# Optimization experiments

Measured on AMD Instinct MI355X. Metric: run time of the kernel, lower is better.

## Reference

```python
import jax, jax.numpy as jnp
import numpy as np

SEQ_LEN = 96      # args.seq_len (in_feats)
H_FEATS = 100
OUT_FEATS = 128
HEADS = 4
K = 64            # args.input_size = nodes per graph
B = 256           # number of graphs (batch_size)
N = K * B
DEG = 8
E = N * DEG
OUT_SIZE = 24     # args.output_size
NEG_SLOPE = 0.2   # PyG GATConv default


def setup_inputs() -> dict:
    key = jax.random.key(0)
    ks = jax.random.split(key, 20)
    s = 0.05
    x = jax.random.normal(ks[0], (N, SEQ_LEN), jnp.float32)
    # intra-graph random edges (dst repeated, src within same graph)
    dst = jnp.repeat(jnp.arange(N, dtype=jnp.int32), DEG)
    src = (dst // K) * K + jax.random.randint(ks[1], (E,), 0, K, dtype=jnp.int32)
    edge_index = jnp.stack([src, dst])
    batch = jnp.repeat(jnp.arange(B, dtype=jnp.int32), K)
    y = jax.random.normal(ks[2], (N, OUT_SIZE), jnp.float32)
    # GATConv 1: in=96 -> heads=4, ch=100
    W1 = jax.random.normal(ks[3], (SEQ_LEN, HEADS * H_FEATS), jnp.float32) * s
    as1 = jax.random.normal(ks[4], (HEADS, H_FEATS), jnp.float32) * s
    ad1 = jax.random.normal(ks[5], (HEADS, H_FEATS), jnp.float32) * s
    b1 = jnp.zeros((H_FEATS,), jnp.float32)
    # GATConv 2: in=100 -> heads=4, ch=128
    W2 = jax.random.normal(ks[6], (H_FEATS, HEADS * OUT_FEATS), jnp.float32) * s
    as2 = jax.random.normal(ks[7], (HEADS, OUT_FEATS), jnp.float32) * s
    ad2 = jax.random.normal(ks[8], (HEADS, OUT_FEATS), jnp.float32) * s
    b2 = jnp.zeros((OUT_FEATS,), jnp.float32)
    # per-node-index MLPs (batched over K)
    fw1 = jax.random.normal(ks[9], (K, OUT_FEATS, 64), jnp.float32) * s
    fb1 = jnp.zeros((K, 64), jnp.float32)
    fw2 = jax.random.normal(ks[10], (K, 64, OUT_SIZE), jnp.float32) * s
    fb2 = jnp.zeros((K, OUT_SIZE), jnp.float32)
    return dict(x=x, edge_index=edge_index, batch=batch, y=y,
                W1=W1, as1=as1, ad1=ad1, b1=b1,
                W2=W2, as2=as2, ad2=ad2, b2=b2,
                fw1=fw1, fb1=fb1, fw2=fw2, fb2=fb2)


def gat_conv(x, src, dst, W, a_src, a_dst, bias):
    # PyG GATConv (concat=False): linear -> per-edge attention -> softmax over
    # incoming edges of each dst -> weighted sum -> mean over heads + bias.
    n = x.shape[0]
    xl = (x @ W).reshape(n, HEADS, -1)                      # [N,H,C]
    al_src = jnp.sum(xl * a_src, axis=-1)                   # [N,H]
    al_dst = jnp.sum(xl * a_dst, axis=-1)                   # [N,H]
    alpha = jax.nn.leaky_relu(al_src[src] + al_dst[dst], NEG_SLOPE)  # [E,H]
    m = jax.ops.segment_max(alpha, dst, num_segments=n)
    ea = jnp.exp(alpha - m[dst])
    denom = jax.ops.segment_sum(ea, dst, num_segments=n)
    w = ea / (denom[dst] + 1e-16)                           # [E,H]
    msg = xl[src] * w[:, :, None]                           # [E,H,C]
    out = jax.ops.segment_sum(msg, dst, num_segments=n)     # [N,H,C]
    return out.mean(axis=1) + bias                          # concat=False


def reference(x, edge_index, batch, y, W1, as1, ad1, b1, W2, as2, ad2, b2, fw1, fb1, fw2, fb2):
    n = x.shape[0]
    src, dst = edge_index[0], edge_index[1]
    loop = jnp.arange(n, dtype=src.dtype)                   # GATConv adds self-loops
    src = jnp.concatenate([src, loop])
    dst = jnp.concatenate([dst, loop])
    h = jax.nn.elu(gat_conv(x, src, dst, W1, as1, ad1, b1))
    h = gat_conv(h, src, dst, W2, as2, ad2, b2)             # [N,128]
    # batch is sorted with K nodes per graph -> stacking == static reshape
    xg = h.reshape(B, K, OUT_FEATS).transpose(1, 0, 2)      # [K,B,128]
    hid = jax.nn.relu(jnp.einsum('kbi,kih->kbh', xg, fw1) + fb1[:, None, :])
    pred = jnp.einsum('kbh,kho->kbo', hid, fw2) + fb2[:, None, :]  # [K,B,out]
    yg = y.reshape(B, K, OUT_SIZE)                          # [B,K,out]
    return pred, yg
```

## Files before the change

### kernel.cpp

```cpp
#include <hip/hip_runtime.h>
#include <hip/hip_bf16.h>
#include <math.h>


#define N_NODES 16384
#define B_GRAPHS 256
#define K_NODES 64
#define DEG 8
#define NHEADS 4
#define C1 100
#define C2 128
#define IN_F 96
#define HID 64
#define OUT_SZ 24
#define PRED_ELEMS (K_NODES * B_GRAPHS * OUT_SZ)

#define W1T_ROWS 448
#define W1T_K    96
#define W2T_ROWS 512
#define W2T_K    128

using bf16 = __hip_bfloat16;
typedef __attribute__((ext_vector_type(8))) short          frag_ab;
typedef __attribute__((ext_vector_type(4))) float          frag_cd;
typedef unsigned short us8 __attribute__((ext_vector_type(8)));
typedef unsigned short us4 __attribute__((ext_vector_type(4)));

__device__ __forceinline__ float us2f(unsigned short u) {
  return __bfloat162float(__ushort_as_bfloat16(u));
}
__device__ __forceinline__ short f2bf_s(float f) {
  return __builtin_bit_cast(short, __float2bfloat16(f));
}

#define P1N (W1T_ROWS * W1T_K)
#define P2N (W2T_ROWS * W2T_K)
#define YG4 (PRED_ELEMS / 4)

__global__ __launch_bounds__(256)
void prep(const float* __restrict__ W1, const float* __restrict__ W2,
          const float* __restrict__ y,
          bf16* __restrict__ W1t, bf16* __restrict__ W2t,
          float* __restrict__ yg) {
  int idx = blockIdx.x * 256 + threadIdx.x;
  if (idx < P1N) {
    int c = idx / W1T_K, k = idx - c * W1T_K;
    W1t[idx] = __float2bfloat16((c < 400) ? W1[(size_t)k * 400 + c] : 0.f);
  } else if (idx < P1N + P2N) {
    int i2 = idx - P1N;
    int c = i2 >> 7, k = i2 & 127;
    W2t[i2] = __float2bfloat16((k < 100) ? W2[(size_t)k * 512 + c] : 0.f);
  } else {
    int j = idx - P1N - P2N;
    if (j < YG4) {
      int i = j * 4;
      float4 v = *(const float4*)(y + i);
      v.x = __bfloat162float(__float2bfloat16(v.x));
      v.y = __bfloat162float(__float2bfloat16(v.y));
      v.z = __bfloat162float(__float2bfloat16(v.z));
      v.w = __bfloat162float(__float2bfloat16(v.w));
      *(float4*)(yg + i) = v;
    }
  }
}

__global__ __launch_bounds__(512)
void gat_fused(const float* __restrict__ x,
               const bf16* __restrict__ W1t, const bf16* __restrict__ W2t,
               const int* __restrict__ esrc,
               const float* __restrict__ as1, const float* __restrict__ ad1,
               const float* __restrict__ b1,
               const float* __restrict__ as2, const float* __restrict__ ad2,
               const float* __restrict__ b2,
               bf16* __restrict__ h2out) {
  constexpr int LDA1 = IN_F + 8;
  constexpr int LDA2 = 136;
  constexpr int LDT  = 72;

  __shared__ __align__(16) short          As[64 * LDA2];
  __shared__ __align__(16) unsigned short xs[512 * LDT];
  __shared__ __align__(16) short          Ps[NHEADS * 64 * LDT];
  __shared__ float avs1[400], avd1[400], avs2[512], avd2[512];
  __shared__ float bia1[C1], bia2[C2];
  __shared__ int   edg[K_NODES * DEG];
  __shared__ float als[64 * 5], ald[64 * 5];

  const int g = blockIdx.x;
  const int t = threadIdx.x;
  const int wv = t >> 6;
  const int l  = t & 63;
  const int lm = l & 15;
  const int lk = (l >> 4) * 8;
  const int rq = (l >> 4) * 4;

  {
    constexpr int QR = IN_F / 4;
    for (int idx = t; idx < 64 * QR; idx += 512) {
      int m = idx / QR, q = idx - m * QR;
      const float4 v = *(const float4*)(x + ((size_t)(g * 64 + m) * IN_F + q * 4));
      short* d = &As[m * LDA1 + q * 4];
      d[0] = f2bf_s(v.x); d[1] = f2bf_s(v.y); d[2] = f2bf_s(v.z); d[3] = f2bf_s(v.w);
    }
  }
  for (int idx = t; idx < 400; idx += 512) { avs1[idx] = as1[idx]; avd1[idx] = ad1[idx]; }
  for (int idx = t; idx < 512; idx += 512) { avs2[idx] = as2[idx]; avd2[idx] = ad2[idx]; }
  if (t < C1) bia1[t] = b1[t];
  if (t < C2) bia2[t] = b2[t];
  if (t < K_NODES * DEG) edg[t] = esrc[g * K_NODES * DEG + t] & (K_NODES - 1);
  for (int idx = t; idx < NHEADS * 64 * LDT / 8; idx += 512)
    *(us8*)&Ps[idx * 8] = (us8)0;
  __syncthreads();

  if (wv < 7) {
    const int n0 = wv * 64;
    frag_cd acc[4][4] = {};
#pragma unroll
    for (int ks = 0; ks < IN_F; ks += 32) {
      frag_ab b[4];
#pragma unroll
      for (int nt = 0; nt < 4; ++nt)
        b[nt] = *(const frag_ab*)((const short*)W1t +
                                  (size_t)(n0 + nt * 16 + lm) * W1T_K + ks + lk);
#pragma unroll
      for (int mt = 0; mt < 4; ++mt) {
        frag_ab a = *(const frag_ab*)&As[(mt * 16 + lm) * LDA1 + ks + lk];
#pragma unroll
        for (int nt = 0; nt < 4; ++nt)
          acc[mt][nt] = __builtin_amdgcn_mfma_f32_16x16x32_bf16(a, b[nt],
                                                                acc[mt][nt], 0, 0, 0);
      }
    }
#pragma unroll
    for (int mt = 0; mt < 4; ++mt)
#pragma unroll
      for (int nt = 0; nt < 4; ++nt) {
        const int c4 = n0 + nt * 16 + lm;
        us4 o;
#pragma unroll
        for (int r = 0; r < 4; ++r) o[r] = (unsigned short)f2bf_s(acc[mt][nt][r]);
        *(us4*)&xs[c4 * LDT + mt * 16 + rq] = o;
      }
  }
  __syncthreads();

  if (t < 256) {
    const int n = t >> 2, h = t & 3;
    float ss = 0.f, sd = 0.f;
#pragma unroll 4
    for (int c = 0; c < C1; ++c) {
      const float v = us2f(xs[(h * C1 + c) * LDT + n]);
      ss += v * avs1[h * C1 + c];
      sd += v * avd1[h * C1 + c];
    }
    als[n * 5 + h] = ss;
    ald[n * 5 + h] = sd;
  }
  __syncthreads();

  if (t < 256) {
    const int n = t >> 2, h = t & 3;
    const float ad = ald[n * 5 + h];
    int   sv[9];
    float a[9];
#pragma unroll
    for (int j = 0; j < 8; ++j) sv[j] = edg[n * DEG + j];
    sv[8] = n;
#pragma unroll
    for (int j = 0; j < 9; ++j) {
      float v = als[sv[j] * 5 + h] + ad;
      a[j] = (v >= 0.f) ? v : 0.2f * v;
    }
    float m = -1e30f;
#pragma unroll
    for (int j = 0; j < 9; ++j) m = fmaxf(m, a[j]);
    float s = 0.f;
#pragma unroll
    for (int j = 0; j < 9; ++j) { a[j] = __expf(a[j] - m); s += a[j]; }
    const float inv = 1.f / (s + 1e-16f);
    short* prow = &Ps[(h * 64 + n) * LDT];
#pragma unroll
    for (int j = 0; j < 9; ++j) {
      float tw = a[j];
#pragma unroll
      for (int i = 0; i < 9; ++i)
        if (i != j && sv[i] == sv[j]) tw += a[i];
      prow[sv[j]] = f2bf_s(tw * inv);
    }
  } else {
    for (int i = t - 256; i < 64 * 28; i += 256) {
      int m = i / 28, kk = 100 + (i - m * 28);
      As[m * LDA2 + kk] = 0;
    }
  }
  __syncthreads();

  {
    const int mw = (wv & 3) * 16;
    const int cg = wv >> 2;
    const int ntb = cg * 4;
    const int nte = (cg == 0) ? 4 : 7;
    frag_cd acc[4] = {};
#pragma unroll
    for (int h = 0; h < NHEADS; ++h)
#pragma unroll
      for (int ks = 0; ks < 64; ks += 32) {
        frag_ab a = *(const frag_ab*)&Ps[(h * 64 + mw + lm) * LDT + ks + lk];
        for (int nt = ntb; nt < nte; ++nt) {
          frag_ab b = *(const frag_ab*)&xs[(h * C1 + nt * 16 + lm) * LDT + ks + lk];
          acc[nt - ntb] = __builtin_amdgcn_mfma_f32_16x16x32_bf16(a, b,
                                                                  acc[nt - ntb], 0, 0, 0);
      }
    }
    for (int nt = ntb; nt < nte; ++nt) {
      const int c = nt * 16 + lm;
      if (c < C1) {
        const float bc = bia1[c];
#pragma unroll
        for (int r = 0; r < 4; ++r) {
          float vv = acc[nt - ntb][r] * 0.25f + bc;
          vv = (vv > 0.f) ? vv : (__expf(vv) - 1.f);
          As[(mw + rq + r) * LDA2 + c] = f2bf_s(vv);
        }
      }
    }
  }
  __syncthreads();

  {
    const int n0 = wv * 64;
    frag_cd acc[4][4] = {};
#pragma unroll
    for (int ks = 0; ks < 128; ks += 32) {
      frag_ab b[4];
#pragma unroll
      for (int nt = 0; nt < 4; ++nt)
        b[nt] = *(const frag_ab*)((const short*)W2t +
                                  (size_t)(n0 + nt * 16 + lm) * W2T_K + ks + lk);
#pragma unroll
      for (int mt = 0; mt < 4; ++mt) {
        frag_ab a = *(const frag_ab*)&As[(mt * 16 + lm) * LDA2 + ks + lk];
#pragma unroll
        for (int nt = 0; nt < 4; ++nt)
          acc[mt][nt] = __builtin_amdgcn_mfma_f32_16x16x32_bf16(a, b[nt],
                                                                acc[mt][nt], 0, 0, 0);
      }
    }
#pragma unroll
    for (int mt = 0; mt < 4; ++mt)
#pragma unroll
      for (int nt = 0; nt < 4; ++nt) {
        const int c4 = n0 + nt * 16 + lm;
        us4 o;
#pragma unroll
        for (int r = 0; r < 4; ++r) o[r] = (unsigned short)f2bf_s(acc[mt][nt][r]);
        *(us4*)&xs[c4 * LDT + mt * 16 + rq] = o;
      }
  }
  __syncthreads();

  if (t < 256) {
    const int n = t >> 2, h = t & 3;
    float ss = 0.f, sd = 0.f;
#pragma unroll 4
    for (int c = 0; c < C2; ++c) {
      const float v = us2f(xs[(h * C2 + c) * LDT + n]);
      ss += v * avs2[h * C2 + c];
      sd += v * avd2[h * C2 + c];
    }
    als[n * 5 + h] = ss;
    ald[n * 5 + h] = sd;
  }
  __syncthreads();

  if (t < 256) {
    const int n = t >> 2, h = t & 3;
    const float ad = ald[n * 5 + h];
    int   sv[9];
    float a[9];
#pragma unroll
    for (int j = 0; j < 8; ++j) sv[j] = edg[n * DEG + j];
    sv[8] = n;
#pragma unroll
    for (int j = 0; j < 9; ++j) {
      float v = als[sv[j] * 5 + h] + ad;
      a[j] = (v >= 0.f) ? v : 0.2f * v;
    }
    float m = -1e30f;
#pragma unroll
    for (int j = 0; j < 9; ++j) m = fmaxf(m, a[j]);
    float s = 0.f;
#pragma unroll
    for (int j = 0; j < 9; ++j) { a[j] = __expf(a[j] - m); s += a[j]; }
    const float inv = 1.f / (s + 1e-16f);
    short* prow = &Ps[(h * 64 + n) * LDT];
#pragma unroll
    for (int j = 0; j < 9; ++j) {
      float tw = a[j];
#pragma unroll
      for (int i = 0; i < 9; ++i)
        if (i != j && sv[i] == sv[j]) tw += a[i];
      prow[sv[j]] = f2bf_s(tw * inv);
    }
  }
  __syncthreads();

  {
    const int mw = (wv & 3) * 16;
    const int cg = wv >> 2;
    const int ntb = cg * 4;
    frag_cd acc[4] = {};
#pragma unroll
    for (int h = 0; h < NHEADS; ++h)
#pragma unroll
      for (int ks = 0; ks < 64; ks += 32) {
        frag_ab a = *(const frag_ab*)&Ps[(h * 64 + mw + lm) * LDT + ks + lk];
#pragma unroll
        for (int nt = 0; nt < 4; ++nt) {
          frag_ab b = *(const frag_ab*)&xs[(h * C2 + (ntb + nt) * 16 + lm) * LDT + ks + lk];
          acc[nt] = __builtin_amdgcn_mfma_f32_16x16x32_bf16(a, b, acc[nt], 0, 0, 0);
        }
      }
    unsigned short* outp = (unsigned short*)h2out + (size_t)(g * 64) * C2;
#pragma unroll
    for (int nt = 0; nt < 4; ++nt) {
      const int c = (ntb + nt) * 16 + lm;
      const float bc = bia2[c];
#pragma unroll
      for (int r = 0; r < 4; ++r) {
        float vv = acc[nt][r] * 0.25f + bc;
        outp[(size_t)(mw + rq + r) * C2 + c] = (unsigned short)f2bf_s(vv);
      }
    }
  }
}

__global__ __launch_bounds__(256)
void mlp_mfma(const bf16* __restrict__ h2,
              const float* __restrict__ fw1, const float* __restrict__ fb1,
              const float* __restrict__ fw2, const float* __restrict__ fb2,
              float* __restrict__ pred) {
  constexpr int LDA = C2 + 8;
  constexpr int LDH = HID + 8;
  __shared__ __align__(16) short As[64 * LDA];
  __shared__ __align__(16) short B1[HID * LDA];
  __shared__ __align__(16) short Hs[64 * LDH];
  __shared__ __align__(16) short B2[32 * LDH];
  __shared__ float b1s[HID];
  __shared__ float b2s[32];

  const int k  = blockIdx.x & 63;
  const int ms = blockIdx.x >> 6;
  const int t  = threadIdx.x;

  for (int idx = t; idx < 64 * 16; idx += 256) {
    int r = idx >> 4, o = idx & 15;
    const us8 v = *(const us8*)((const unsigned short*)h2 +
        ((size_t)((ms * 64 + r) * K_NODES + k) * C2) + o * 8);
    *(us8*)&As[r * LDA + o * 8] = v;
  }
  for (int idx = t; idx < C2 * HID; idx += 256) {
    int kk = idx >> 6, n = idx & 63;
    B1[n * LDA + kk] = f2bf_s(fw1[(size_t)k * C2 * HID + kk * HID + n]);
  }
  for (int idx = t; idx < HID * 32; idx += 256) {
    int kk = idx >> 5, n = idx & 31;
    float v = (n < OUT_SZ) ? fw2[(size_t)k * HID * OUT_SZ + kk * OUT_SZ + n] : 0.f;
    B2[n * LDH + kk] = f2bf_s(v);
  }
  if (t < HID) b1s[t] = fb1[k * HID + t];
  if (t < 32)  b2s[t] = (t < OUT_SZ) ? fb2[k * OUT_SZ + t] : 0.f;
  __syncthreads();

  const int wv = t >> 6;
  const int l  = t & 63;
  const int lm = l & 15;
  const int lk = (l >> 4) * 8;
  const int rq = (l >> 4) * 4;

  frag_cd acc[4] = {};
#pragma unroll
  for (int ks = 0; ks < C2; ks += 32) {
    frag_ab a = *(const frag_ab*)&As[(wv * 16 + lm) * LDA + ks + lk];
#pragma unroll
    for (int nt = 0; nt < 4; ++nt) {
      frag_ab b = *(const frag_ab*)&B1[(nt * 16 + lm) * LDA + ks + lk];
      acc[nt] = __builtin_amdgcn_mfma_f32_16x16x32_bf16(a, b, acc[nt], 0, 0, 0);
    }
  }
#pragma unroll
  for (int nt = 0; nt < 4; ++nt) {
    const int j  = nt * 16 + lm;
    const float bj = b1s[j];
#pragma unroll
    for (int r = 0; r < 4; ++r) {
      const int m = wv * 16 + rq + r;
      Hs[m * LDH + j] = f2bf_s(fmaxf(acc[nt][r] + bj, 0.f));
    }
  }
  __syncthreads();

  frag_cd acc2[2] = {};
#pragma unroll
  for (int ks = 0; ks < HID; ks += 32) {
    frag_ab a = *(const frag_ab*)&Hs[(wv * 16 + lm) * LDH + ks + lk];
#pragma unroll
    for (int nt = 0; nt < 2; ++nt) {
      frag_ab b = *(const frag_ab*)&B2[(nt * 16 + lm) * LDH + ks + lk];
      acc2[nt] = __builtin_amdgcn_mfma_f32_16x16x32_bf16(a, b, acc2[nt], 0, 0, 0);
    }
  }
#pragma unroll
  for (int nt = 0; nt < 2; ++nt) {
    const int q = nt * 16 + lm;
    if (q < OUT_SZ) {
      const float bq = b2s[q];
#pragma unroll
      for (int r = 0; r < 4; ++r) {
        const int m = wv * 16 + rq + r;
        pred[((size_t)k * B_GRAPHS + ms * 64 + m) * OUT_SZ + q] = acc2[nt][r] + bq;
      }
    }
  }
}

extern "C" void kernel_launch(void* const* d_in, const int* in_sizes, int n_in,
                              void* d_out, int out_size, void* d_ws, size_t ws_size,
                              hipStream_t stream) {
  const float* x   = (const float*)d_in[0];
  const int*   ei  = (const int*)d_in[1];
  const float* y   = (const float*)d_in[3];
  const float* W1  = (const float*)d_in[4];
  const float* as1 = (const float*)d_in[5];
  const float* ad1 = (const float*)d_in[6];
  const float* b1  = (const float*)d_in[7];
  const float* W2  = (const float*)d_in[8];
  const float* as2 = (const float*)d_in[9];
  const float* ad2 = (const float*)d_in[10];
  const float* b2  = (const float*)d_in[11];
  const float* fw1 = (const float*)d_in[12];
  const float* fb1 = (const float*)d_in[13];
  const float* fw2 = (const float*)d_in[14];
  const float* fb2 = (const float*)d_in[15];

  bf16* h2  = (bf16*)d_ws;
  bf16* W1t = h2 + (size_t)N_NODES * C2;
  bf16* W2t = W1t + P1N;

  float* out = (float*)d_out;

  prep<<<(P1N + P2N + YG4 + 255) / 256, 256, 0, stream>>>(
      W1, W2, y, W1t, W2t, out + PRED_ELEMS);

  gat_fused<<<B_GRAPHS, 512, 0, stream>>>(x, W1t, W2t, ei,
                                          as1, ad1, b1, as2, ad2, b2, h2);

  mlp_mfma<<<K_NODES * 4, 256, 0, stream>>>(h2, fw1, fb1, fw2, fb2, out);
}
```

Baseline: 119.4 us.

## Fold attention vectors into weight GEMMs and pre-transpose MLP weights to bf16

Precomputes W·a_src and W·a_dst as extra columns appended to the transposed weight matrices, so the attention logits come out of the existing MFMA GEMMs. This replaces the separate per-node dot-product loops and two block barriers per layer. The MLP weights are converted and transposed to bf16 once in the prep kernel. The GAT output is written in a [K,B,C] layout so the MLP kernel reads A and B fragments straight from global memory without staging them in LDS. The trade-offs are that the logits are now rounded to bf16 before the softmax, and the prep kernel does more work.

```diff
diff --git a/kernel.cpp b/kernel.cpp
--- a/kernel.cpp
+++ b/kernel.cpp
@@ -17,7 +17,7 @@
 
 #define W1T_ROWS 448
 #define W1T_K    96
-#define W2T_ROWS 512
+#define W2T_ROWS 528
 #define W2T_K    128
 
 using bf16 = __hip_bfloat16;
@@ -33,33 +33,73 @@
   return __builtin_bit_cast(short, __float2bfloat16(f));
 }
 
-#define P1N (W1T_ROWS * W1T_K)
-#define P2N (W2T_ROWS * W2T_K)
-#define YG4 (PRED_ELEMS / 4)
+#define P1N  (W1T_ROWS * W1T_K)
+#define P2N  (W2T_ROWS * W2T_K)
+#define YG4  (PRED_ELEMS / 4)
+#define FW1N (K_NODES * HID * C2)
+#define FW2N (K_NODES * 32 * HID)
+#define PREP_TOT (P1N + P2N + YG4 + FW1N + FW2N)
 
 __global__ __launch_bounds__(256)
 void prep(const float* __restrict__ W1, const float* __restrict__ W2,
           const float* __restrict__ y,
+          const float* __restrict__ as1, const float* __restrict__ ad1,
+          const float* __restrict__ as2, const float* __restrict__ ad2,
+          const float* __restrict__ fw1, const float* __restrict__ fw2,
           bf16* __restrict__ W1t, bf16* __restrict__ W2t,
+          bf16* __restrict__ fw1t, bf16* __restrict__ fw2t,
           float* __restrict__ yg) {
   int idx = blockIdx.x * 256 + threadIdx.x;
   if (idx < P1N) {
     int c = idx / W1T_K, k = idx - c * W1T_K;
-    W1t[idx] = __float2bfloat16((c < 400) ? W1[(size_t)k * 400 + c] : 0.f);
+    float v = 0.f;
+    if (c < 400) {
+      v = W1[(size_t)k * 400 + c];
+    } else if (c < 408) {
+      int h = (c - 400) & 3;
+      const float* av = (c < 404) ? as1 : ad1;
+      float s = 0.f;
+#pragma unroll 4
+      for (int q = 0; q < 100; ++q)
+        s += W1[(size_t)k * 400 + h * 100 + q] * av[h * 100 + q];
+      v = s;
+    }
+    W1t[idx] = __float2bfloat16(v);
   } else if (idx < P1N + P2N) {
     int i2 = idx - P1N;
-    int c = i2 >> 7, k = i2 & 127;
-    W2t[i2] = __float2bfloat16((k < 100) ? W2[(size_t)k * 512 + c] : 0.f);
+    int c = i2 >> 7, kk = i2 & 127;
+    float v = 0.f;
+    if (c < 512) {
+      if (kk < 100) v = W2[(size_t)kk * 512 + c];
+    } else if (c < 520 && kk < 100) {
+      int h = (c - 512) & 3;
+      const float* av = (c < 516) ? as2 : ad2;
+      float s = 0.f;
+#pragma unroll 4
+      for (int q = 0; q < 128; ++q)
+        s += W2[(size_t)kk * 512 + h * 128 + q] * av[h * 128 + q];
+      v = s;
+    }
+    W2t[i2] = __float2bfloat16(v);
+  } else if (idx < P1N + P2N + YG4) {
+    int j = idx - P1N - P2N;
+    int i = j * 4;
+    float4 v = *(const float4*)(y + i);
+    v.x = __bfloat162float(__float2bfloat16(v.x));
+    v.y = __bfloat162float(__float2bfloat16(v.y));
+    v.z = __bfloat162float(__float2bfloat16(v.z));
+    v.w = __bfloat162float(__float2bfloat16(v.w));
+    *(float4*)(yg + i) = v;
+  } else if (idx < P1N + P2N + YG4 + FW1N) {
+    int i4 = idx - (P1N + P2N + YG4);
+    int k = i4 >> 13, r = i4 & 8191, n = r >> 7, kk = r & 127;
+    fw1t[i4] = __float2bfloat16(fw1[(size_t)k * (C2 * HID) + kk * HID + n]);
   } else {
-    int j = idx - P1N - P2N;
-    if (j < YG4) {
-      int i = j * 4;
-      float4 v = *(const float4*)(y + i);
-      v.x = __bfloat162float(__float2bfloat16(v.x));
-      v.y = __bfloat162float(__float2bfloat16(v.y));
-      v.z = __bfloat162float(__float2bfloat16(v.z));
-      v.w = __bfloat162float(__float2bfloat16(v.w));
-      *(float4*)(yg + i) = v;
+    int i5 = idx - (P1N + P2N + YG4 + FW1N);
+    if (i5 < FW2N) {
+      int k = i5 >> 11, r = i5 & 2047, n = r >> 6, kk = r & 63;
+      fw2t[i5] = __float2bfloat16(
+          (n < OUT_SZ) ? fw2[(size_t)k * (HID * OUT_SZ) + kk * OUT_SZ + n] : 0.f);
     }
   }
 }
@@ -68,22 +108,17 @@
 void gat_fused(const float* __restrict__ x,
                const bf16* __restrict__ W1t, const bf16* __restrict__ W2t,
                const int* __restrict__ esrc,
-               const float* __restrict__ as1, const float* __restrict__ ad1,
-               const float* __restrict__ b1,
-               const float* __restrict__ as2, const float* __restrict__ ad2,
-               const float* __restrict__ b2,
-               bf16* __restrict__ h2out) {
+               const float* __restrict__ b1, const float* __restrict__ b2,
+               bf16* __restrict__ h2t) {
   constexpr int LDA1 = IN_F + 8;
   constexpr int LDA2 = 136;
   constexpr int LDT  = 72;
 
   __shared__ __align__(16) short          As[64 * LDA2];
-  __shared__ __align__(16) unsigned short xs[512 * LDT];
+  __shared__ __align__(16) unsigned short xs[W2T_ROWS * LDT];
   __shared__ __align__(16) short          Ps[NHEADS * 64 * LDT];
-  __shared__ float avs1[400], avd1[400], avs2[512], avd2[512];
   __shared__ float bia1[C1], bia2[C2];
   __shared__ int   edg[K_NODES * DEG];
-  __shared__ float als[64 * 5], ald[64 * 5];
 
   const int g = blockIdx.x;
   const int t = threadIdx.x;
@@ -102,10 +137,8 @@
       d[0] = f2bf_s(v.x); d[1] = f2bf_s(v.y); d[2] = f2bf_s(v.z); d[3] = f2bf_s(v.w);
     }
   }
-  for (int idx = t; idx < 400; idx += 512) { avs1[idx] = as1[idx]; avd1[idx] = ad1[idx]; }
-  for (int idx = t; idx < 512; idx += 512) { avs2[idx] = as2[idx]; avd2[idx] = ad2[idx]; }
   if (t < C1) bia1[t] = b1[t];
-  if (t < C2) bia2[t] = b2[t];
+  else if (t >= 128 && t < 128 + C2) bia2[t - 128] = b2[t - 128];
   if (t < K_NODES * DEG) edg[t] = esrc[g * K_NODES * DEG + t] & (K_NODES - 1);
   for (int idx = t; idx < NHEADS * 64 * LDT / 8; idx += 512)
     *(us8*)&Ps[idx * 8] = (us8)0;
@@ -145,21 +178,7 @@
 
   if (t < 256) {
     const int n = t >> 2, h = t & 3;
-    float ss = 0.f, sd = 0.f;
-#pragma unroll 4
-    for (int c = 0; c < C1; ++c) {
-      const float v = us2f(xs[(h * C1 + c) * LDT + n]);
-      ss += v * avs1[h * C1 + c];
-      sd += v * avd1[h * C1 + c];
-    }
-    als[n * 5 + h] = ss;
-    ald[n * 5 + h] = sd;
-  }
-  __syncthreads();
-
-  if (t < 256) {
-    const int n = t >> 2, h = t & 3;
-    const float ad = ald[n * 5 + h];
+    const float ad = us2f(xs[(404 + h) * LDT + n]);
     int   sv[9];
     float a[9];
 #pragma unroll
@@ -167,7 +186,7 @@
     sv[8] = n;
 #pragma unroll
     for (int j = 0; j < 9; ++j) {
-      float v = als[sv[j] * 5 + h] + ad;
+      float v = us2f(xs[(400 + h) * LDT + sv[j]]) + ad;
       a[j] = (v >= 0.f) ? v : 0.2f * v;
     }
     float m = -1e30f;
@@ -229,6 +248,7 @@
   {
     const int n0 = wv * 64;
     frag_cd acc[4][4] = {};
+    frag_cd accL[4] = {};
 #pragma unroll
     for (int ks = 0; ks < 128; ks += 32) {
       frag_ab b[4];
@@ -236,6 +256,10 @@
       for (int nt = 0; nt < 4; ++nt)
         b[nt] = *(const frag_ab*)((const short*)W2t +
                                   (size_t)(n0 + nt * 16 + lm) * W2T_K + ks + lk);
+      frag_ab bl;
+      if (wv == 0)
+        bl = *(const frag_ab*)((const short*)W2t +
+                               (size_t)(512 + lm) * W2T_K + ks + lk);
 #pragma unroll
       for (int mt = 0; mt < 4; ++mt) {
         frag_ab a = *(const frag_ab*)&As[(mt * 16 + lm) * LDA2 + ks + lk];
@@ -243,6 +267,8 @@
         for (int nt = 0; nt < 4; ++nt)
           acc[mt][nt] = __builtin_amdgcn_mfma_f32_16x16x32_bf16(a, b[nt],
                                                                 acc[mt][nt], 0, 0, 0);
+        if (wv == 0)
+          accL[mt] = __builtin_amdgcn_mfma_f32_16x16x32_bf16(a, bl, accL[mt], 0, 0, 0);
       }
     }
 #pragma unroll
@@ -255,26 +281,21 @@
         for (int r = 0; r < 4; ++r) o[r] = (unsigned short)f2bf_s(acc[mt][nt][r]);
         *(us4*)&xs[c4 * LDT + mt * 16 + rq] = o;
       }
+    if (wv == 0) {
+#pragma unroll
+      for (int mt = 0; mt < 4; ++mt) {
+        us4 o;
+#pragma unroll
+        for (int r = 0; r < 4; ++r) o[r] = (unsigned short)f2bf_s(accL[mt][r]);
+        *(us4*)&xs[(512 + lm) * LDT + mt * 16 + rq] = o;
+      }
+    }
   }
   __syncthreads();
 
   if (t < 256) {
     const int n = t >> 2, h = t & 3;
-    float ss = 0.f, sd = 0.f;
-#pragma unroll 4
-    for (int c = 0; c < C2; ++c) {
-      const float v = us2f(xs[(h * C2 + c) * LDT + n]);
-      ss += v * avs2[h * C2 + c];
-      sd += v * avd2[h * C2 + c];
-    }
-    als[n * 5 + h] = ss;
-    ald[n * 5 + h] = sd;
-  }
-  __syncthreads();
-
-  if (t < 256) {
-    const int n = t >> 2, h = t & 3;
-    const float ad = ald[n * 5 + h];
+    const float ad = us2f(xs[(516 + h) * LDT + n]);
     int   sv[9];
     float a[9];
 #pragma unroll
@@ -282,7 +303,7 @@
     sv[8] = n;
 #pragma unroll
     for (int j = 0; j < 9; ++j) {
-      float v = als[sv[j] * 5 + h] + ad;
+      float v = us2f(xs[(512 + h) * LDT + sv[j]]) + ad;
       a[j] = (v >= 0.f) ? v : 0.2f * v;
     }
     float m = -1e30f;
@@ -320,7 +341,7 @@
           acc[nt] = __builtin_amdgcn_mfma_f32_16x16x32_bf16(a, b, acc[nt], 0, 0, 0);
         }
       }
-    unsigned short* outp = (unsigned short*)h2out + (size_t)(g * 64) * C2;
+    unsigned short* outp = (unsigned short*)h2t;
 #pragma unroll
     for (int nt = 0; nt < 4; ++nt) {
       const int c = (ntb + nt) * 16 + lm;
@@ -328,69 +349,48 @@
 #pragma unroll
       for (int r = 0; r < 4; ++r) {
         float vv = acc[nt][r] * 0.25f + bc;
-        outp[(size_t)(mw + rq + r) * C2 + c] = (unsigned short)f2bf_s(vv);
+        outp[((size_t)(mw + rq + r) * B_GRAPHS + g) * C2 + c] =
+            (unsigned short)f2bf_s(vv);
       }
     }
   }
 }
 
 __global__ __launch_bounds__(256)
-void mlp_mfma(const bf16* __restrict__ h2,
-              const float* __restrict__ fw1, const float* __restrict__ fb1,
-              const float* __restrict__ fw2, const float* __restrict__ fb2,
+void mlp_mfma(const bf16* __restrict__ h2t,
+              const bf16* __restrict__ fw1t, const float* __restrict__ fb1,
+              const bf16* __restrict__ fw2t, const float* __restrict__ fb2,
               float* __restrict__ pred) {
-  constexpr int LDA = C2 + 8;
   constexpr int LDH = HID + 8;
-  __shared__ __align__(16) short As[64 * LDA];
-  __shared__ __align__(16) short B1[HID * LDA];
   __shared__ __align__(16) short Hs[64 * LDH];
-  __shared__ __align__(16) short B2[32 * LDH];
-  __shared__ float b1s[HID];
-  __shared__ float b2s[32];
 
   const int k  = blockIdx.x & 63;
   const int ms = blockIdx.x >> 6;
   const int t  = threadIdx.x;
-
-  for (int idx = t; idx < 64 * 16; idx += 256) {
-    int r = idx >> 4, o = idx & 15;
-    const us8 v = *(const us8*)((const unsigned short*)h2 +
-        ((size_t)((ms * 64 + r) * K_NODES + k) * C2) + o * 8);
-    *(us8*)&As[r * LDA + o * 8] = v;
-  }
-  for (int idx = t; idx < C2 * HID; idx += 256) {
-    int kk = idx >> 6, n = idx & 63;
-    B1[n * LDA + kk] = f2bf_s(fw1[(size_t)k * C2 * HID + kk * HID + n]);
-  }
-  for (int idx = t; idx < HID * 32; idx += 256) {
-    int kk = idx >> 5, n = idx & 31;
-    float v = (n < OUT_SZ) ? fw2[(size_t)k * HID * OUT_SZ + kk * OUT_SZ + n] : 0.f;
-    B2[n * LDH + kk] = f2bf_s(v);
-  }
-  if (t < HID) b1s[t] = fb1[k * HID + t];
-  if (t < 32)  b2s[t] = (t < OUT_SZ) ? fb2[k * OUT_SZ + t] : 0.f;
-  __syncthreads();
-
   const int wv = t >> 6;
   const int l  = t & 63;
   const int lm = l & 15;
   const int lk = (l >> 4) * 8;
   const int rq = (l >> 4) * 4;
 
+  const unsigned short* A  = (const unsigned short*)h2t +
+                             ((size_t)k * B_GRAPHS + ms * 64) * C2;
+  const unsigned short* B1 = (const unsigned short*)fw1t + (size_t)k * (HID * C2);
+
   frag_cd acc[4] = {};
 #pragma unroll
   for (int ks = 0; ks < C2; ks += 32) {
-    frag_ab a = *(const frag_ab*)&As[(wv * 16 + lm) * LDA + ks + lk];
+    frag_ab a = *(const frag_ab*)(A + (size_t)(wv * 16 + lm) * C2 + ks + lk);
 #pragma unroll
     for (int nt = 0; nt < 4; ++nt) {
-      frag_ab b = *(const frag_ab*)&B1[(nt * 16 + lm) * LDA + ks + lk];
+      frag_ab b = *(const frag_ab*)(B1 + (size_t)(nt * 16 + lm) * C2 + ks + lk);
       acc[nt] = __builtin_amdgcn_mfma_f32_16x16x32_bf16(a, b, acc[nt], 0, 0, 0);
     }
   }
 #pragma unroll
   for (int nt = 0; nt < 4; ++nt) {
     const int j  = nt * 16 + lm;
-    const float bj = b1s[j];
+    const float bj = fb1[k * HID + j];
 #pragma unroll
     for (int r = 0; r < 4; ++r) {
       const int m = wv * 16 + rq + r;
@@ -399,13 +399,14 @@
   }
   __syncthreads();
 
+  const unsigned short* B2 = (const unsigned short*)fw2t + (size_t)k * (32 * HID);
   frag_cd acc2[2] = {};
 #pragma unroll
   for (int ks = 0; ks < HID; ks += 32) {
     frag_ab a = *(const frag_ab*)&Hs[(wv * 16 + lm) * LDH + ks + lk];
 #pragma unroll
     for (int nt = 0; nt < 2; ++nt) {
-      frag_ab b = *(const frag_ab*)&B2[(nt * 16 + lm) * LDH + ks + lk];
+      frag_ab b = *(const frag_ab*)(B2 + (size_t)(nt * 16 + lm) * HID + ks + lk);
       acc2[nt] = __builtin_amdgcn_mfma_f32_16x16x32_bf16(a, b, acc2[nt], 0, 0, 0);
     }
   }
@@ -413,7 +414,7 @@
   for (int nt = 0; nt < 2; ++nt) {
     const int q = nt * 16 + lm;
     if (q < OUT_SZ) {
-      const float bq = b2s[q];
+      const float bq = fb2[k * OUT_SZ + q];
 #pragma unroll
       for (int r = 0; r < 4; ++r) {
         const int m = wv * 16 + rq + r;
@@ -442,17 +443,19 @@
   const float* fw2 = (const float*)d_in[14];
   const float* fb2 = (const float*)d_in[15];
 
-  bf16* h2  = (bf16*)d_ws;
-  bf16* W1t = h2 + (size_t)N_NODES * C2;
-  bf16* W2t = W1t + P1N;
+  bf16* h2t  = (bf16*)d_ws;
+  bf16* W1t  = h2t + (size_t)N_NODES * C2;
+  bf16* W2t  = W1t + P1N;
+  bf16* fw1t = W2t + P2N;
+  bf16* fw2t = fw1t + FW1N;
 
   float* out = (float*)d_out;
 
-  prep<<<(P1N + P2N + YG4 + 255) / 256, 256, 0, stream>>>(
-      W1, W2, y, W1t, W2t, out + PRED_ELEMS);
-
-  gat_fused<<<B_GRAPHS, 512, 0, stream>>>(x, W1t, W2t, ei,
-                                          as1, ad1, b1, as2, ad2, b2, h2);
-
-  mlp_mfma<<<K_NODES * 4, 256, 0, stream>>>(h2, fw1, fb1, fw2, fb2, out);
-}
+  prep<<<(PREP_TOT + 255) / 256, 256, 0, stream>>>(
+      W1, W2, y, as1, ad1, as2, ad2, fw1, fw2, W1t, W2t, fw1t, fw2t,
+      out + PRED_ELEMS);
+
+  gat_fused<<<B_GRAPHS, 512, 0, stream>>>(x, W1t, W2t, ei, b1, b2, h2t);
+
+  mlp_mfma<<<K_NODES * 4, 256, 0, stream>>>(h2t, fw1t, fb1, fw2t, fb2, out);
+}
```

Measured after the change: 118.5 us. About the same (-0.7%).
